# Optimization experiments

Measured on AMD Instinct MI355X. Metric: run time of the kernel, lower is better.

Reference implementation:

```python
import jax, jax.numpy as jnp
import numpy as np

B, L = 32, 128
NUM_LANG, NUM_WORD, NUM_POS, NUM_DEP, NUM_ENT, NUM_IOB = 5, 50000, 50, 50, 20, 4
LANG_D, WORD_D, POS_D, DEP_D, ENT_D, IOB_D = 50, 300, 50, 50, 50, 50
IN_D = LANG_D + WORD_D + POS_D + DEP_D + ENT_D + IOB_D  # 550
H = 200  # lstm_dim // 2 per direction
PAD_IDX, STOP_IDX = 0, 2


def setup_inputs() -> dict:
    key = jax.random.key(0)
    ks = jax.random.split(key, 24)
    f32 = jnp.float32
    w = lambda k, shape: jax.random.normal(k, shape, f32) * 0.05
    e = lambda k, n, d: jax.random.normal(k, (n, d), f32) * 0.1
    return {
        # word idxs in [3, NUM_WORD) so no PAD(0)/STOP(2): all sentences full length
        'lang_idxs': jax.random.randint(ks[0], (B, L), 0, NUM_LANG),
        'word_idxs': jax.random.randint(ks[1], (B, L), 3, NUM_WORD),
        'pos_idxs': jax.random.randint(ks[2], (B, L), 1, NUM_POS),
        'dep_idxs': jax.random.randint(ks[3], (B, L), 1, NUM_DEP),
        'ent_idxs': jax.random.randint(ks[4], (B, L), 1, NUM_ENT),
        'ent_iob_idxs': jax.random.randint(ks[5], (B, L), 1, NUM_IOB),
        'E_lang': e(ks[6], NUM_LANG, LANG_D),
        'E_word': e(ks[7], NUM_WORD, WORD_D),
        'E_pos': e(ks[8], NUM_POS, POS_D),
        'E_dep': e(ks[9], NUM_DEP, DEP_D),
        'E_ent': e(ks[10], NUM_ENT, ENT_D),
        'E_iob': e(ks[11], NUM_IOB, IOB_D),
        # biLSTM params, leading dim 2 = direction (0 fwd, 1 bwd); torch gate order i,f,g,o
        'Wih0': w(ks[12], (2, 4 * H, IN_D)),
        'Whh0': w(ks[13], (2, 4 * H, H)),
        'bih0': w(ks[14], (2, 4 * H)),
        'bhh0': w(ks[15], (2, 4 * H)),
        'Wih1': w(ks[16], (2, 4 * H, 2 * H)),
        'Whh1': w(ks[17], (2, 4 * H, H)),
        'bih1': w(ks[18], (2, 4 * H)),
        'bhh1': w(ks[19], (2, 4 * H)),
    }


def _lstm_dir(x, Wi, Wh, bi, bh, reverse):
    # x: (L, B, in) time-major; single direction LSTM
    xg = jnp.einsum('lbi,gi->lbg', x, Wi) + (bi + bh)  # precompute input gates

    def step(carry, xt):
        h, c = carry
        g = xt + h @ Wh.T
        i, f, gg, o = jnp.split(g, 4, axis=-1)
        c = jax.nn.sigmoid(f) * c + jax.nn.sigmoid(i) * jnp.tanh(gg)
        h = jax.nn.sigmoid(o) * jnp.tanh(c)
        return (h, c), h

    nb = x.shape[1]
    h0 = jnp.zeros((nb, Wh.shape[-1]), x.dtype)
    _, hs = jax.lax.scan(step, (h0, h0), xg, reverse=reverse)
    return hs  # (L, B, H), in original time order


def _bilstm_layer(x, Wih, Whh, bih, bhh):
    fwd = _lstm_dir(x, Wih[0], Whh[0], bih[0], bhh[0], False)
    bwd = _lstm_dir(x, Wih[1], Whh[1], bih[1], bhh[1], True)
    return jnp.concatenate([fwd, bwd], axis=-1)  # (L, B, 2H)


def reference(lang_idxs, word_idxs, pos_idxs, dep_idxs, ent_idxs, ent_iob_idxs,
              E_lang, E_word, E_pos, E_dep, E_ent, E_iob,
              Wih0, Whh0, bih0, bhh0, Wih1, Whh1, bih1, bhh1):
    mask = word_idxs != PAD_IDX            # (B, L); all True for these inputs
    sen_lens = mask.sum(1)                 # all == L, so sort/pack/pad are no-ops
    emb = jnp.concatenate([E_lang[lang_idxs], E_word[word_idxs], E_pos[pos_idxs],
                           E_dep[dep_idxs], E_ent[ent_idxs], E_iob[ent_iob_idxs]], axis=-1)
    # emb_drop disabled (eval mode)
    x = jnp.transpose(emb, (1, 0, 2))      # (L, B, IN_D)
    x = _bilstm_layer(x, Wih0, Whh0, bih0, bhh0)
    x = _bilstm_layer(x, Wih1, Whh1, bih1, bhh1)   # inter-layer dropout disabled
    h = jnp.transpose(x, (1, 0, 2))        # (B, L, 2H)
    f, bw = h[..., :H], h[..., H:]
    # pairwise span features: x[i,j] = h_i - h_j masked by triu(1) on [0, L-1)
    a, b = np.triu_indices(L - 1, 1)       # static: (L-1)(L-2)/2 spans, row-major in (a,b)
    span_f = f[:, b] - f[:, a]             # forward half: f_b - f_a
    span_b = bw[:, a + 1] - bw[:, b + 1]   # backward half: bw_{a+1} - bw_{b+1}
    x_span = jnp.concatenate([span_f, span_b], axis=-1)  # (B, 8001, 2H)
    return (x_span, sen_lens - 2)
```

## Files before the change

### kernel.cpp

```cpp
#include <hip/hip_runtime.h>
#include <hip/hip_bf16.h>
#include <hip/hip_fp16.h>


typedef unsigned short u16;
typedef unsigned int u32;
typedef short shortx8 __attribute__((ext_vector_type(8)));
typedef float floatx4 __attribute__((ext_vector_type(4)));
typedef _Float16 half2v __attribute__((ext_vector_type(2)));

#define B_ 32
#define L_ 128
#define H_ 200
#define K0P 576
#define K1P 416
#define NG 1600
#define NPAIR 8001
#define SPAN_ELEMS 102412800

__device__ __forceinline__ float bf2f(u16 v) {
  u32 u = ((u32)v) << 16;
  return __builtin_bit_cast(float, u);
}
__device__ __forceinline__ u16 f2bf(float f) {
  __hip_bfloat16 h = __float2bfloat16(f);
  return __builtin_bit_cast(u16, h);
}
__device__ __forceinline__ float loadF(const void* p, int idx, int isf32) {
  return isf32 ? ((const float*)p)[idx] : bf2f(((const u16*)p)[idx]);
}
__device__ __forceinline__ float dot2h(u32 w, u32 h, float acc) {
#if __has_builtin(__builtin_amdgcn_fdot2)
  return __builtin_amdgcn_fdot2(__builtin_bit_cast(half2v, w),
                                __builtin_bit_cast(half2v, h), acc, false);
#else
  half2v a = __builtin_bit_cast(half2v, w), b = __builtin_bit_cast(half2v, h);
  return acc + (float)a.x * (float)b.x + (float)a.y * (float)b.y;
#endif
}
__device__ __forceinline__ float sigf(float x) { return 1.f / (1.f + __expf(-x)); }
__device__ __forceinline__ float tanhff(float x) {
  x = fminf(fmaxf(x, -15.f), 15.f);
  float e = __expf(-2.f * x);
  return (1.f - e) / (1.f + e);
}


__global__ void prep_kernel(const void* __restrict__ Ew, const int* __restrict__ word,
                            int* __restrict__ flag, int* __restrict__ pa, int* __restrict__ pb,
                            void* __restrict__ out) {
  __shared__ int sflag;
  int tid = threadIdx.x;
  if (tid == 0) {
    const u16* p = (const u16*)Ew;
    int big = 0;
    for (int i = 0; i < 128; ++i) {
      int e = (p[i] >> 7) & 0xFF;
      if (e >= 0x84) big++;
    }
    int f = (big >= 4) ? 1 : 0;
    *flag = f;
    sflag = f;
  }
  if (tid < 126) {
    int a = tid;
    int off = a * 126 - a * (a - 1) / 2;
    for (int b = a + 1; b <= 126; ++b) {
      pa[off] = a;
      pb[off] = b;
      ++off;
    }
  }
  __syncthreads();
  if (tid >= 128 && tid < 128 + B_) {
    int b = tid - 128;
    int cnt = 0;
    for (int l = 0; l < L_; ++l) cnt += (word[b * L_ + l] != 0);
    float v = (float)(cnt - 2);
    if (sflag) ((float*)out)[SPAN_ELEMS + b] = v;
    else ((u16*)out)[SPAN_ELEMS + b] = f2bf(v);
  }
}


__global__ void embed_kernel(const int* __restrict__ lang, const int* __restrict__ word,
                             const int* __restrict__ pos, const int* __restrict__ dep,
                             const int* __restrict__ ent, const int* __restrict__ iob,
                             const void* __restrict__ El, const void* __restrict__ Ew,
                             const void* __restrict__ Ep, const void* __restrict__ Ed,
                             const void* __restrict__ Ee, const void* __restrict__ Ei,
                             u16* __restrict__ x0, const int* __restrict__ flag) {
  int row = blockIdx.x;
  int isf32 = *flag;
  int l = row >> 5, b = row & 31;
  int io = b * L_ + l;
  int li = lang[io], wi = word[io], pi = pos[io], di = dep[io], ei = ent[io], ii = iob[io];
  for (int c = threadIdx.x; c < K0P; c += 64) {
    float v = 0.f;
    if (c < 50) v = loadF(El, li * 50 + c, isf32);
    else if (c < 350) v = loadF(Ew, wi * 300 + (c - 50), isf32);
    else if (c < 400) v = loadF(Ep, pi * 50 + (c - 350), isf32);
    else if (c < 450) v = loadF(Ed, di * 50 + (c - 400), isf32);
    else if (c < 500) v = loadF(Ee, ei * 50 + (c - 450), isf32);
    else if (c < 550) v = loadF(Ei, ii * 50 + (c - 500), isf32);
    x0[row * K0P + c] = f2bf(v);
  }
}


__global__ void pack_kernel(const void* __restrict__ Wih0, const void* __restrict__ Whh0,
                            const void* __restrict__ bih0, const void* __restrict__ bhh0,
                            const void* __restrict__ Wih1, const void* __restrict__ Whh1,
                            const void* __restrict__ bih1, const void* __restrict__ bhh1,
                            u16* __restrict__ Wc0, u16* __restrict__ Wc1,
                            float* __restrict__ bias0, float* __restrict__ bias1,
                            u16* __restrict__ Whf, u16* __restrict__ x1,
                            const int* __restrict__ flag) {
  int idx = blockIdx.x * 256 + threadIdx.x;
  int isf32 = *flag;
  if (idx < 1600 * K0P) {
    int r = idx / K0P, c = idx - r * K0P;
    Wc0[idx] = (c < 550) ? f2bf(loadF(Wih0, r * 550 + c, isf32)) : (u16)0;
    return;
  }
  idx -= 1600 * K0P;
  if (idx < 1600 * K1P) {
    int r = idx / K1P, c = idx - r * K1P;
    Wc1[idx] = (c < 400) ? f2bf(loadF(Wih1, r * 400 + c, isf32)) : (u16)0;
    return;
  }
  idx -= 1600 * K1P;
  if (idx < 1600) { bias0[idx] = loadF(bih0, idx, isf32) + loadF(bhh0, idx, isf32); return; }
  idx -= 1600;
  if (idx < 1600) { bias1[idx] = loadF(bih1, idx, isf32) + loadF(bhh1, idx, isf32); return; }
  idx -= 1600;
  if (idx < 640000) {
    float s = (idx < 320000) ? loadF(Whh0, idx, isf32) : loadF(Whh1, idx - 320000, isf32);
    _Float16 h = (_Float16)s;
    Whf[idx] = __builtin_bit_cast(u16, h);
    return;
  }
  idx -= 640000;
  if (idx < 4096 * 16) {
    int row = idx >> 4, c = idx & 15;
    x1[row * K1P + 400 + c] = 0;
  }
}


__global__ __launch_bounds__(256) void gemm_bt(const u16* __restrict__ A, const u16* __restrict__ W,
                                               const float* __restrict__ bias, u16* __restrict__ C,
                                               int Ks) {
  __shared__ __align__(16) u16 As[64 * 40];
  __shared__ __align__(16) u16 Bs[64 * 40];
  int tid = threadIdx.x;
  int n0 = blockIdx.x * 64, m0 = blockIdx.y * 64;
  int lane = tid & 63, wv = tid >> 6, ln = lane & 15, quad = lane >> 4;
  floatx4 acc[4] = {{0.f, 0.f, 0.f, 0.f}, {0.f, 0.f, 0.f, 0.f}, {0.f, 0.f, 0.f, 0.f}, {0.f, 0.f, 0.f, 0.f}};
  int arow = tid >> 2, acs = (tid & 3) * 8;
  const u16* Ag = A + (size_t)(m0 + arow) * Ks + acs;
  const u16* Wg = W + (size_t)(n0 + arow) * Ks + acs;
  for (int k0 = 0; k0 < Ks; k0 += 32) {
    __syncthreads();
    *(uint4*)&As[arow * 40 + acs] = *(const uint4*)(Ag + k0);
    *(uint4*)&Bs[arow * 40 + acs] = *(const uint4*)(Wg + k0);
    __syncthreads();
    shortx8 af = *(const shortx8*)&As[(wv * 16 + ln) * 40 + quad * 8];
    shortx8 b0 = *(const shortx8*)&Bs[(ln) * 40 + quad * 8];
    shortx8 b1 = *(const shortx8*)&Bs[(16 + ln) * 40 + quad * 8];
    shortx8 b2 = *(const shortx8*)&Bs[(32 + ln) * 40 + quad * 8];
    shortx8 b3 = *(const shortx8*)&Bs[(48 + ln) * 40 + quad * 8];
    acc[0] = __builtin_amdgcn_mfma_f32_16x16x32_bf16(af, b0, acc[0], 0, 0, 0);
    acc[1] = __builtin_amdgcn_mfma_f32_16x16x32_bf16(af, b1, acc[1], 0, 0, 0);
    acc[2] = __builtin_amdgcn_mfma_f32_16x16x32_bf16(af, b2, acc[2], 0, 0, 0);
    acc[3] = __builtin_amdgcn_mfma_f32_16x16x32_bf16(af, b3, acc[3], 0, 0, 0);
  }
  int rbase = m0 + wv * 16 + quad * 4;
#pragma unroll
  for (int ns = 0; ns < 4; ++ns) {
    int cg = n0 + ns * 16 + ln;
    float bv = bias[cg];
#pragma unroll
    for (int r = 0; r < 4; ++r) {
      C[(size_t)(rbase + r) * NG + cg] = f2bf(acc[ns][r] + bv);
    }
  }
}


__global__ __launch_bounds__(448, 2) void rec_kernel(const u16* __restrict__ xg, const u16* __restrict__ Whf,
                                                     int layer, u16* __restrict__ x1, float* __restrict__ hs) {
  int tid = threadIdx.x;
  int batch = blockIdx.x >> 1, dir = blockIdx.x & 1;
  __shared__ __align__(16) u16 hsh[H_];
  __shared__ float gsh[800];
  uint4 wA[25], wB[25];
  if (tid < 400) {
    const uint4* wa = (const uint4*)(Whf + (size_t)((layer * 2 + dir) * 800 + tid) * 200);
    const uint4* wb = (const uint4*)(Whf + (size_t)((layer * 2 + dir) * 800 + tid + 400) * 200);
#pragma unroll
    for (int i = 0; i < 25; ++i) { wA[i] = wa[i]; wB[i] = wb[i]; }
  }
  float cst = 0.f;
  if (tid < H_) hsh[tid] = 0;
  int rstep = (dir ? -B_ : B_) * NG;
  const u16* xr = xg + (size_t)((dir ? (L_ - 1) * B_ : 0) + batch) * NG + dir * 800;
  float a0 = 0.f, a1 = 0.f;
  if (tid < 400) { a0 = bf2f(xr[tid]); a1 = bf2f(xr[tid + 400]); }
  __syncthreads();
  for (int t = 0; t < L_; ++t) {
    int tt = dir ? (L_ - 1 - t) : t;
    float n0 = 0.f, n1 = 0.f;
    if (tid < 400) {
      if (t + 1 < L_) {
        const u16* xn = xr + (ptrdiff_t)(t + 1) * rstep;
        n0 = bf2f(xn[tid]);
        n1 = bf2f(xn[tid + 400]);
      }
      float c0 = 0.f, c1 = 0.f;
      const uint4* hv4 = (const uint4*)hsh;
#pragma unroll
      for (int kk = 0; kk < 25; kk += 2) {
        uint4 hv = hv4[kk];
        a0 = dot2h(wA[kk].x, hv.x, a0);
        a0 = dot2h(wA[kk].y, hv.y, a0);
        a0 = dot2h(wA[kk].z, hv.z, a0);
        a0 = dot2h(wA[kk].w, hv.w, a0);
        a1 = dot2h(wB[kk].x, hv.x, a1);
        a1 = dot2h(wB[kk].y, hv.y, a1);
        a1 = dot2h(wB[kk].z, hv.z, a1);
        a1 = dot2h(wB[kk].w, hv.w, a1);
        if (kk + 1 < 25) {
          uint4 hw = hv4[kk + 1];
          c0 = dot2h(wA[kk + 1].x, hw.x, c0);
          c0 = dot2h(wA[kk + 1].y, hw.y, c0);
          c0 = dot2h(wA[kk + 1].z, hw.z, c0);
          c0 = dot2h(wA[kk + 1].w, hw.w, c0);
          c1 = dot2h(wB[kk + 1].x, hw.x, c1);
          c1 = dot2h(wB[kk + 1].y, hw.y, c1);
          c1 = dot2h(wB[kk + 1].z, hw.z, c1);
          c1 = dot2h(wB[kk + 1].w, hw.w, c1);
        }
      }
      gsh[tid] = a0 + c0;
      gsh[tid + 400] = a1 + c1;
    }
    __syncthreads();
    if (tid < H_) {
      float gi = gsh[tid], gf = gsh[200 + tid], gg = gsh[400 + tid], go = gsh[600 + tid];
      cst = sigf(gf) * cst + sigf(gi) * tanhff(gg);
      float h = sigf(go) * tanhff(cst);
      _Float16 hh = (_Float16)h;
      hsh[tid] = __builtin_bit_cast(u16, hh);
      int orow = tt * B_ + batch;
      if (layer == 0) {
        x1[(size_t)orow * K1P + dir * H_ + tid] = f2bf(h);
      } else {
        hs[(size_t)orow * 400 + dir * H_ + tid] = h;
      }
    }
    a0 = n0;
    a1 = n1;
    __syncthreads();
  }
}


__global__ __launch_bounds__(256) void span_kernel(const float* __restrict__ hs, const int* __restrict__ pa,
                                                   const int* __restrict__ pb, void* __restrict__ outp,
                                                   const int* __restrict__ flag) {
  int bb = blockIdx.y;
  int p0 = blockIdx.x * 64;
  int isf32 = *flag;
  for (int idx = threadIdx.x; idx < 64 * 50; idx += 256) {
    int pr = idx / 50;
    int q = idx - pr * 50;
    int p = p0 + pr;
    if (p >= NPAIR) continue;
    int a = pa[p], b = pb[p];
    int fwd = (q < 25);
    int r1 = fwd ? b : (a + 1);
    int r2 = fwd ? a : (b + 1);
    int col = q * 8;
    const float4* h1 = (const float4*)(hs + (size_t)(r1 * B_ + bb) * 400 + col);
    const float4* h2 = (const float4*)(hs + (size_t)(r2 * B_ + bb) * 400 + col);
    float4 x0 = h1[0], x1v = h1[1], y0 = h2[0], y1 = h2[1];
    float4 d0 = make_float4(x0.x - y0.x, x0.y - y0.y, x0.z - y0.z, x0.w - y0.w);
    float4 d1 = make_float4(x1v.x - y1.x, x1v.y - y1.y, x1v.z - y1.z, x1v.w - y1.w);
    if (isf32) {
      float4* o = (float4*)outp + (size_t)(bb * NPAIR + p) * 100 + q * 2;
      o[0] = d0;
      o[1] = d1;
    } else {
      u32 w0 = (u32)f2bf(d0.x) | ((u32)f2bf(d0.y) << 16);
      u32 w1 = (u32)f2bf(d0.z) | ((u32)f2bf(d0.w) << 16);
      u32 w2 = (u32)f2bf(d1.x) | ((u32)f2bf(d1.y) << 16);
      u32 w3 = (u32)f2bf(d1.z) | ((u32)f2bf(d1.w) << 16);
      ((uint4*)outp)[(size_t)(bb * NPAIR + p) * 50 + q] = make_uint4(w0, w1, w2, w3);
    }
  }
}


extern "C" void kernel_launch(void* const* d_in, const int* in_sizes, int n_in,
                              void* d_out, int out_size, void* d_ws, size_t ws_size,
                              hipStream_t stream) {
  const int* lang = (const int*)d_in[0];
  const int* word = (const int*)d_in[1];
  const int* pos = (const int*)d_in[2];
  const int* dep = (const int*)d_in[3];
  const int* ent = (const int*)d_in[4];
  const int* iob = (const int*)d_in[5];

  char* ws = (char*)d_ws;
  int* flag = (int*)(ws + 0);
  int* pa = (int*)(ws + 4096);
  int* pb = (int*)(ws + 36864);
  u16* x0 = (u16*)(ws + 69632);
  u16* Wc0 = (u16*)(ws + 4788224);
  u16* Wc1 = (u16*)(ws + 6631424);
  float* bias0 = (float*)(ws + 7962624);
  float* bias1 = (float*)(ws + 7969024);
  u16* Whf = (u16*)(ws + 7975424);
  u16* x1 = (u16*)(ws + 9255424);
  float* hs1 = (float*)(ws + 12663296);
  u16* xg = (u16*)(ws + 19216896);

  hipLaunchKernelGGL(prep_kernel, dim3(1), dim3(256), 0, stream, d_in[7], word, flag, pa, pb, d_out);
  hipLaunchKernelGGL(embed_kernel, dim3(4096), dim3(64), 0, stream,
                     lang, word, pos, dep, ent, iob,
                     d_in[6], d_in[7], d_in[8], d_in[9], d_in[10], d_in[11], x0, flag);
  hipLaunchKernelGGL(pack_kernel, dim3(8969), dim3(256), 0, stream,
                     d_in[12], d_in[13], d_in[14], d_in[15],
                     d_in[16], d_in[17], d_in[18], d_in[19],
                     Wc0, Wc1, bias0, bias1, Whf, x1, flag);
  hipLaunchKernelGGL(gemm_bt, dim3(25, 64), dim3(256), 0, stream, x0, Wc0, bias0, xg, K0P);
  hipLaunchKernelGGL(rec_kernel, dim3(64), dim3(448), 0, stream, xg, Whf, 0, x1, hs1);
  hipLaunchKernelGGL(gemm_bt, dim3(25, 64), dim3(256), 0, stream, x1, Wc1, bias1, xg, K1P);
  hipLaunchKernelGGL(rec_kernel, dim3(64), dim3(448), 0, stream, xg, Whf, 1, x1, hs1);
  hipLaunchKernelGGL(span_kernel, dim3(126, 32), dim3(256), 0, stream, hs1, pa, pb, d_out, flag);
}
```

Measured before the change: 965.2 us.

## Fuse setup kernels, double-buffer GEMM K-loop, nontemporal span stores

Merges the prep, embed and pack kernels into one setup launch, with each block sniffing the dtype itself. The GEMM now uses a 64-wide K step with register prefetch of the next tile, and x1's K padding is widened to 448 so it can reuse the x0 buffer. The padding columns of x1 are now zeroed inside the recurrent kernel. The span kernel swaps its grid order so batch is the fast block dimension and writes its large output with nontemporal stores. The aim is to cut launch overhead, GEMM sync stalls and cache pollution from the output write, at the cost of redundant dtype sniffing in every block and more layout coupling between kernels.

```diff
diff --git a/kernel.cpp b/kernel.cpp
--- a/kernel.cpp
+++ b/kernel.cpp
@@ -7,16 +7,22 @@
 typedef unsigned int u32;
 typedef short shortx8 __attribute__((ext_vector_type(8)));
 typedef float floatx4 __attribute__((ext_vector_type(4)));
+typedef float fx4 __attribute__((ext_vector_type(4)));
+typedef unsigned int ux4 __attribute__((ext_vector_type(4)));
 typedef _Float16 half2v __attribute__((ext_vector_type(2)));
 
 #define B_ 32
 #define L_ 128
 #define H_ 200
 #define K0P 576
-#define K1P 416
+#define K1P 448
 #define NG 1600
 #define NPAIR 8001
 #define SPAN_ELEMS 102412800
+
+#define EMB_BLKS 1024
+#define PACK_ELEMS (1600 * K0P + 1600 * K1P + 1600 + 1600 + 640000)
+#define PACK_BLKS ((PACK_ELEMS + 255) / 256)
 
 __device__ __forceinline__ float bf2f(u16 v) {
   u32 u = ((u32)v) << 16;
@@ -45,23 +51,81 @@
   return (1.f - e) / (1.f + e);
 }
 
-
-__global__ void prep_kernel(const void* __restrict__ Ew, const int* __restrict__ word,
-                            int* __restrict__ flag, int* __restrict__ pa, int* __restrict__ pb,
-                            void* __restrict__ out) {
-  __shared__ int sflag;
-  int tid = threadIdx.x;
-  if (tid == 0) {
-    const u16* p = (const u16*)Ew;
-    int big = 0;
-    for (int i = 0; i < 128; ++i) {
-      int e = (p[i] >> 7) & 0xFF;
-      if (e >= 0x84) big++;
-    }
-    int f = (big >= 4) ? 1 : 0;
-    *flag = f;
-    sflag = f;
-  }
+__device__ __forceinline__ int sniff(const u16* p) {
+  int big = 0;
+#pragma unroll 16
+  for (int i = 0; i < 128; ++i) {
+    int e = (p[i] >> 7) & 0xFF;
+    big += (e >= 0x84);
+  }
+  return (big >= 4) ? 1 : 0;
+}
+
+
+__global__ void setup_kernel(const int* __restrict__ lang, const int* __restrict__ word,
+                             const int* __restrict__ pos, const int* __restrict__ dep,
+                             const int* __restrict__ ent, const int* __restrict__ iob,
+                             const void* __restrict__ El, const void* __restrict__ Ew,
+                             const void* __restrict__ Ep, const void* __restrict__ Ed,
+                             const void* __restrict__ Ee, const void* __restrict__ Ei,
+                             const void* __restrict__ Wih0, const void* __restrict__ Whh0,
+                             const void* __restrict__ bih0, const void* __restrict__ bhh0,
+                             const void* __restrict__ Wih1, const void* __restrict__ Whh1,
+                             const void* __restrict__ bih1, const void* __restrict__ bhh1,
+                             u16* __restrict__ x0, u16* __restrict__ Wc0, u16* __restrict__ Wc1,
+                             float* __restrict__ bias0, float* __restrict__ bias1,
+                             u16* __restrict__ Whf, int* __restrict__ flag,
+                             int* __restrict__ pa, int* __restrict__ pb, void* __restrict__ out) {
+  int blk = blockIdx.x, tid = threadIdx.x;
+  int isf32 = sniff((const u16*)Ew);
+
+  if (blk < EMB_BLKS) {
+    int row = blk * 4 + (tid >> 6);
+    int lane = tid & 63;
+    int l = row >> 5, b = row & 31;
+    int io = b * L_ + l;
+    int li = lang[io], wi = word[io], pi = pos[io], di = dep[io], ei = ent[io], ii = iob[io];
+    for (int c = lane; c < K0P; c += 64) {
+      float v = 0.f;
+      if (c < 50) v = loadF(El, li * 50 + c, isf32);
+      else if (c < 350) v = loadF(Ew, wi * 300 + (c - 50), isf32);
+      else if (c < 400) v = loadF(Ep, pi * 50 + (c - 350), isf32);
+      else if (c < 450) v = loadF(Ed, di * 50 + (c - 400), isf32);
+      else if (c < 500) v = loadF(Ee, ei * 50 + (c - 450), isf32);
+      else if (c < 550) v = loadF(Ei, ii * 50 + (c - 500), isf32);
+      x0[row * K0P + c] = f2bf(v);
+    }
+    return;
+  }
+  blk -= EMB_BLKS;
+
+  if (blk < PACK_BLKS) {
+    int idx = blk * 256 + tid;
+    if (idx < 1600 * K0P) {
+      int r = idx / K0P, c = idx - r * K0P;
+      Wc0[idx] = (c < 550) ? f2bf(loadF(Wih0, r * 550 + c, isf32)) : (u16)0;
+      return;
+    }
+    idx -= 1600 * K0P;
+    if (idx < 1600 * K1P) {
+      int r = idx / K1P, c = idx - r * K1P;
+      Wc1[idx] = (c < 400) ? f2bf(loadF(Wih1, r * 400 + c, isf32)) : (u16)0;
+      return;
+    }
+    idx -= 1600 * K1P;
+    if (idx < 1600) { bias0[idx] = loadF(bih0, idx, isf32) + loadF(bhh0, idx, isf32); return; }
+    idx -= 1600;
+    if (idx < 1600) { bias1[idx] = loadF(bih1, idx, isf32) + loadF(bhh1, idx, isf32); return; }
+    idx -= 1600;
+    if (idx < 640000) {
+      float s = (idx < 320000) ? loadF(Whh0, idx, isf32) : loadF(Whh1, idx - 320000, isf32);
+      _Float16 h = (_Float16)s;
+      Whf[idx] = __builtin_bit_cast(u16, h);
+    }
+    return;
+  }
+
+  if (tid == 0) *flag = isf32;
   if (tid < 126) {
     int a = tid;
     int off = a * 126 - a * (a - 1) / 2;
@@ -71,79 +135,13 @@
       ++off;
     }
   }
-  __syncthreads();
   if (tid >= 128 && tid < 128 + B_) {
     int b = tid - 128;
     int cnt = 0;
     for (int l = 0; l < L_; ++l) cnt += (word[b * L_ + l] != 0);
     float v = (float)(cnt - 2);
-    if (sflag) ((float*)out)[SPAN_ELEMS + b] = v;
+    if (isf32) ((float*)out)[SPAN_ELEMS + b] = v;
     else ((u16*)out)[SPAN_ELEMS + b] = f2bf(v);
-  }
-}
-
-
-__global__ void embed_kernel(const int* __restrict__ lang, const int* __restrict__ word,
-                             const int* __restrict__ pos, const int* __restrict__ dep,
-                             const int* __restrict__ ent, const int* __restrict__ iob,
-                             const void* __restrict__ El, const void* __restrict__ Ew,
-                             const void* __restrict__ Ep, const void* __restrict__ Ed,
-                             const void* __restrict__ Ee, const void* __restrict__ Ei,
-                             u16* __restrict__ x0, const int* __restrict__ flag) {
-  int row = blockIdx.x;
-  int isf32 = *flag;
-  int l = row >> 5, b = row & 31;
-  int io = b * L_ + l;
-  int li = lang[io], wi = word[io], pi = pos[io], di = dep[io], ei = ent[io], ii = iob[io];
-  for (int c = threadIdx.x; c < K0P; c += 64) {
-    float v = 0.f;
-    if (c < 50) v = loadF(El, li * 50 + c, isf32);
-    else if (c < 350) v = loadF(Ew, wi * 300 + (c - 50), isf32);
-    else if (c < 400) v = loadF(Ep, pi * 50 + (c - 350), isf32);
-    else if (c < 450) v = loadF(Ed, di * 50 + (c - 400), isf32);
-    else if (c < 500) v = loadF(Ee, ei * 50 + (c - 450), isf32);
-    else if (c < 550) v = loadF(Ei, ii * 50 + (c - 500), isf32);
-    x0[row * K0P + c] = f2bf(v);
-  }
-}
-
-
-__global__ void pack_kernel(const void* __restrict__ Wih0, const void* __restrict__ Whh0,
-                            const void* __restrict__ bih0, const void* __restrict__ bhh0,
-                            const void* __restrict__ Wih1, const void* __restrict__ Whh1,
-                            const void* __restrict__ bih1, const void* __restrict__ bhh1,
-                            u16* __restrict__ Wc0, u16* __restrict__ Wc1,
-                            float* __restrict__ bias0, float* __restrict__ bias1,
-                            u16* __restrict__ Whf, u16* __restrict__ x1,
-                            const int* __restrict__ flag) {
-  int idx = blockIdx.x * 256 + threadIdx.x;
-  int isf32 = *flag;
-  if (idx < 1600 * K0P) {
-    int r = idx / K0P, c = idx - r * K0P;
-    Wc0[idx] = (c < 550) ? f2bf(loadF(Wih0, r * 550 + c, isf32)) : (u16)0;
-    return;
-  }
-  idx -= 1600 * K0P;
-  if (idx < 1600 * K1P) {
-    int r = idx / K1P, c = idx - r * K1P;
-    Wc1[idx] = (c < 400) ? f2bf(loadF(Wih1, r * 400 + c, isf32)) : (u16)0;
-    return;
-  }
-  idx -= 1600 * K1P;
-  if (idx < 1600) { bias0[idx] = loadF(bih0, idx, isf32) + loadF(bhh0, idx, isf32); return; }
-  idx -= 1600;
-  if (idx < 1600) { bias1[idx] = loadF(bih1, idx, isf32) + loadF(bhh1, idx, isf32); return; }
-  idx -= 1600;
-  if (idx < 640000) {
-    float s = (idx < 320000) ? loadF(Whh0, idx, isf32) : loadF(Whh1, idx - 320000, isf32);
-    _Float16 h = (_Float16)s;
-    Whf[idx] = __builtin_bit_cast(u16, h);
-    return;
-  }
-  idx -= 640000;
-  if (idx < 4096 * 16) {
-    int row = idx >> 4, c = idx & 15;
-    x1[row * K1P + 400 + c] = 0;
   }
 }
 
@@ -151,8 +149,8 @@
 __global__ __launch_bounds__(256) void gemm_bt(const u16* __restrict__ A, const u16* __restrict__ W,
                                                const float* __restrict__ bias, u16* __restrict__ C,
                                                int Ks) {
-  __shared__ __align__(16) u16 As[64 * 40];
-  __shared__ __align__(16) u16 Bs[64 * 40];
+  __shared__ __align__(16) u16 As[64 * 72];
+  __shared__ __align__(16) u16 Bs[64 * 72];
   int tid = threadIdx.x;
   int n0 = blockIdx.x * 64, m0 = blockIdx.y * 64;
   int lane = tid & 63, wv = tid >> 6, ln = lane & 15, quad = lane >> 4;
@@ -160,20 +158,38 @@
   int arow = tid >> 2, acs = (tid & 3) * 8;
   const u16* Ag = A + (size_t)(m0 + arow) * Ks + acs;
   const u16* Wg = W + (size_t)(n0 + arow) * Ks + acs;
-  for (int k0 = 0; k0 < Ks; k0 += 32) {
+  int asb = arow * 72 + acs;
+  uint4 ra0 = *(const uint4*)(Ag);
+  uint4 ra1 = *(const uint4*)(Ag + 32);
+  uint4 rb0 = *(const uint4*)(Wg);
+  uint4 rb1 = *(const uint4*)(Wg + 32);
+  for (int k0 = 0; k0 < Ks; k0 += 64) {
+    *(uint4*)&As[asb] = ra0;
+    *(uint4*)&As[asb + 32] = ra1;
+    *(uint4*)&Bs[asb] = rb0;
+    *(uint4*)&Bs[asb + 32] = rb1;
     __syncthreads();
-    *(uint4*)&As[arow * 40 + acs] = *(const uint4*)(Ag + k0);
-    *(uint4*)&Bs[arow * 40 + acs] = *(const uint4*)(Wg + k0);
+    if (k0 + 64 < Ks) {
+      ra0 = *(const uint4*)(Ag + k0 + 64);
+      ra1 = *(const uint4*)(Ag + k0 + 96);
+      rb0 = *(const uint4*)(Wg + k0 + 64);
+      rb1 = *(const uint4*)(Wg + k0 + 96);
+    }
+    int abase = (wv * 16 + ln) * 72;
+#pragma unroll
+    for (int ks = 0; ks < 2; ++ks) {
+      int ko = ks * 32 + quad * 8;
+      shortx8 af = *(const shortx8*)&As[abase + ko];
+      shortx8 b0 = *(const shortx8*)&Bs[ln * 72 + ko];
+      shortx8 b1 = *(const shortx8*)&Bs[(16 + ln) * 72 + ko];
+      shortx8 b2 = *(const shortx8*)&Bs[(32 + ln) * 72 + ko];
+      shortx8 b3 = *(const shortx8*)&Bs[(48 + ln) * 72 + ko];
+      acc[0] = __builtin_amdgcn_mfma_f32_16x16x32_bf16(af, b0, acc[0], 0, 0, 0);
+      acc[1] = __builtin_amdgcn_mfma_f32_16x16x32_bf16(af, b1, acc[1], 0, 0, 0);
+      acc[2] = __builtin_amdgcn_mfma_f32_16x16x32_bf16(af, b2, acc[2], 0, 0, 0);
+      acc[3] = __builtin_amdgcn_mfma_f32_16x16x32_bf16(af, b3, acc[3], 0, 0, 0);
+    }
     __syncthreads();
-    shortx8 af = *(const shortx8*)&As[(wv * 16 + ln) * 40 + quad * 8];
-    shortx8 b0 = *(const shortx8*)&Bs[(ln) * 40 + quad * 8];
-    shortx8 b1 = *(const shortx8*)&Bs[(16 + ln) * 40 + quad * 8];
-    shortx8 b2 = *(const shortx8*)&Bs[(32 + ln) * 40 + quad * 8];
-    shortx8 b3 = *(const shortx8*)&Bs[(48 + ln) * 40 + quad * 8];
-    acc[0] = __builtin_amdgcn_mfma_f32_16x16x32_bf16(af, b0, acc[0], 0, 0, 0);
-    acc[1] = __builtin_amdgcn_mfma_f32_16x16x32_bf16(af, b1, acc[1], 0, 0, 0);
-    acc[2] = __builtin_amdgcn_mfma_f32_16x16x32_bf16(af, b2, acc[2], 0, 0, 0);
-    acc[3] = __builtin_amdgcn_mfma_f32_16x16x32_bf16(af, b3, acc[3], 0, 0, 0);
   }
   int rbase = m0 + wv * 16 + quad * 4;
 #pragma unroll
@@ -246,18 +262,20 @@
       gsh[tid + 400] = a1 + c1;
     }
     __syncthreads();
+    int orow = tt * B_ + batch;
     if (tid < H_) {
       float gi = gsh[tid], gf = gsh[200 + tid], gg = gsh[400 + tid], go = gsh[600 + tid];
       cst = sigf(gf) * cst + sigf(gi) * tanhff(gg);
       float h = sigf(go) * tanhff(cst);
       _Float16 hh = (_Float16)h;
       hsh[tid] = __builtin_bit_cast(u16, hh);
-      int orow = tt * B_ + batch;
       if (layer == 0) {
         x1[(size_t)orow * K1P + dir * H_ + tid] = f2bf(h);
       } else {
         hs[(size_t)orow * 400 + dir * H_ + tid] = h;
       }
+    } else if (layer == 0 && tid >= 256 && tid < 256 + 48) {
+      x1[(size_t)orow * K1P + 400 + (tid - 256)] = (u16)0;
     }
     a0 = n0;
     a1 = n1;
@@ -269,8 +287,8 @@
 __global__ __launch_bounds__(256) void span_kernel(const float* __restrict__ hs, const int* __restrict__ pa,
                                                    const int* __restrict__ pb, void* __restrict__ outp,
                                                    const int* __restrict__ flag) {
-  int bb = blockIdx.y;
-  int p0 = blockIdx.x * 64;
+  int bb = blockIdx.x;
+  int p0 = blockIdx.y * 64;
   int isf32 = *flag;
   for (int idx = threadIdx.x; idx < 64 * 50; idx += 256) {
     int pr = idx / 50;
@@ -282,21 +300,21 @@
     int r1 = fwd ? b : (a + 1);
     int r2 = fwd ? a : (b + 1);
     int col = q * 8;
-    const float4* h1 = (const float4*)(hs + (size_t)(r1 * B_ + bb) * 400 + col);
-    const float4* h2 = (const float4*)(hs + (size_t)(r2 * B_ + bb) * 400 + col);
-    float4 x0 = h1[0], x1v = h1[1], y0 = h2[0], y1 = h2[1];
-    float4 d0 = make_float4(x0.x - y0.x, x0.y - y0.y, x0.z - y0.z, x0.w - y0.w);
-    float4 d1 = make_float4(x1v.x - y1.x, x1v.y - y1.y, x1v.z - y1.z, x1v.w - y1.w);
+    const fx4* h1 = (const fx4*)(hs + (size_t)(r1 * B_ + bb) * 400 + col);
+    const fx4* h2 = (const fx4*)(hs + (size_t)(r2 * B_ + bb) * 400 + col);
+    fx4 d0 = h1[0] - h2[0];
+    fx4 d1 = h1[1] - h2[1];
     if (isf32) {
-      float4* o = (float4*)outp + (size_t)(bb * NPAIR + p) * 100 + q * 2;
-      o[0] = d0;
-      o[1] = d1;
+      fx4* o = (fx4*)outp + (size_t)(bb * NPAIR + p) * 100 + q * 2;
+      __builtin_nontemporal_store(d0, o);
+      __builtin_nontemporal_store(d1, o + 1);
     } else {
-      u32 w0 = (u32)f2bf(d0.x) | ((u32)f2bf(d0.y) << 16);
-      u32 w1 = (u32)f2bf(d0.z) | ((u32)f2bf(d0.w) << 16);
-      u32 w2 = (u32)f2bf(d1.x) | ((u32)f2bf(d1.y) << 16);
-      u32 w3 = (u32)f2bf(d1.z) | ((u32)f2bf(d1.w) << 16);
-      ((uint4*)outp)[(size_t)(bb * NPAIR + p) * 50 + q] = make_uint4(w0, w1, w2, w3);
+      ux4 w;
+      w.x = (u32)f2bf(d0.x) | ((u32)f2bf(d0.y) << 16);
+      w.y = (u32)f2bf(d0.z) | ((u32)f2bf(d0.w) << 16);
+      w.z = (u32)f2bf(d1.x) | ((u32)f2bf(d1.y) << 16);
+      w.w = (u32)f2bf(d1.z) | ((u32)f2bf(d1.w) << 16);
+      __builtin_nontemporal_store(w, (ux4*)outp + (size_t)(bb * NPAIR + p) * 50 + q);
     }
   }
 }
@@ -317,26 +335,24 @@
   int* pa = (int*)(ws + 4096);
   int* pb = (int*)(ws + 36864);
   u16* x0 = (u16*)(ws + 69632);
+  u16* x1 = x0;
   u16* Wc0 = (u16*)(ws + 4788224);
   u16* Wc1 = (u16*)(ws + 6631424);
-  float* bias0 = (float*)(ws + 7962624);
-  float* bias1 = (float*)(ws + 7969024);
-  u16* Whf = (u16*)(ws + 7975424);
-  u16* x1 = (u16*)(ws + 9255424);
-  float* hs1 = (float*)(ws + 12663296);
-  u16* xg = (u16*)(ws + 19216896);
-
-  hipLaunchKernelGGL(prep_kernel, dim3(1), dim3(256), 0, stream, d_in[7], word, flag, pa, pb, d_out);
-  hipLaunchKernelGGL(embed_kernel, dim3(4096), dim3(64), 0, stream,
+  float* bias0 = (float*)(ws + 8065024);
+  float* bias1 = (float*)(ws + 8071424);
+  u16* Whf = (u16*)(ws + 8077824);
+  float* hs1 = (float*)(ws + 9357824);
+  u16* xg = (u16*)(ws + 15911424);
+
+  hipLaunchKernelGGL(setup_kernel, dim3(EMB_BLKS + PACK_BLKS + 1), dim3(256), 0, stream,
                      lang, word, pos, dep, ent, iob,
-                     d_in[6], d_in[7], d_in[8], d_in[9], d_in[10], d_in[11], x0, flag);
-  hipLaunchKernelGGL(pack_kernel, dim3(8969), dim3(256), 0, stream,
+                     d_in[6], d_in[7], d_in[8], d_in[9], d_in[10], d_in[11],
                      d_in[12], d_in[13], d_in[14], d_in[15],
                      d_in[16], d_in[17], d_in[18], d_in[19],
-                     Wc0, Wc1, bias0, bias1, Whf, x1, flag);
+                     x0, Wc0, Wc1, bias0, bias1, Whf, flag, pa, pb, d_out);
   hipLaunchKernelGGL(gemm_bt, dim3(25, 64), dim3(256), 0, stream, x0, Wc0, bias0, xg, K0P);
   hipLaunchKernelGGL(rec_kernel, dim3(64), dim3(448), 0, stream, xg, Whf, 0, x1, hs1);
   hipLaunchKernelGGL(gemm_bt, dim3(25, 64), dim3(256), 0, stream, x1, Wc1, bias1, xg, K1P);
   hipLaunchKernelGGL(rec_kernel, dim3(64), dim3(448), 0, stream, xg, Whf, 1, x1, hs1);
-  hipLaunchKernelGGL(span_kernel, dim3(126, 32), dim3(256), 0, stream, hs1, pa, pb, d_out, flag);
-}
+  hipLaunchKernelGGL(span_kernel, dim3(32, 126), dim3(256), 0, stream, hs1, pa, pb, d_out, flag);
+}
```

New measurement: 1.019 ms. 5.5% more time.
